# Optimization experiments

Measured on AMD Instinct MI355X. Metric: run time of the kernel, lower is better.

## Reference

```python
import jax, jax.numpy as jnp
import numpy as np

KERNEL = 5
PADDING = 2
STRIDE = 2
MIXTURES = 2
OUT_CH = 128


def setup_inputs() -> dict:
    key = jax.random.key(0)
    ks = jax.random.split(key, 7)
    B, CIN, H, W = 8, 64, 128, 128
    return {
        "x": jax.random.normal(ks[0], (B, CIN, H, W), jnp.float32),
        "w_q": jax.random.normal(ks[1], (OUT_CH, CIN), jnp.float32) * 0.05,
        "w_k": jax.random.normal(ks[2], (OUT_CH, CIN), jnp.float32) * 0.05,
        "w_v": jax.random.normal(ks[3], (OUT_CH * MIXTURES, CIN), jnp.float32) * 0.05,
        "row_emb": jax.random.normal(ks[4], (OUT_CH, KERNEL), jnp.float32),
        "col_emb": jax.random.normal(ks[5], (OUT_CH, KERNEL), jnp.float32),
        "mix_emb": jax.random.normal(ks[6], (OUT_CH, MIXTURES), jnp.float32),
    }


def _patches(t, stride):
    # im2col, matching torch nn.Unfold channel-major ordering: [B, C*k*k, Ho, Wo]
    return jax.lax.conv_general_dilated_patches(
        t, (KERNEL, KERNEL), (stride, stride),
        padding=[(PADDING, PADDING), (PADDING, PADDING)])


def reference(x, w_q, w_k, w_v, row_emb, col_emb, mix_emb):
    K2 = KERNEL * KERNEL
    # 1x1 convolutions (groups=1, no bias)
    q = jnp.einsum('bchw,oc->bohw', x, w_q)            # [B,C,H,W]
    k = jnp.einsum('bchw,oc->bohw', x, w_k)            # [B,C,H,W]
    v = jnp.einsum('bchw,oc->bohw', x, w_v)            # [B,C*M,H,W]

    # key patches: [B, C, K2, Ho, Wo]
    kp = _patches(k, STRIDE)
    B, _, Ho, Wo = kp.shape
    kp = kp.reshape(B, OUT_CH, K2, Ho, Wo)

    # queries at strided output locations (unfold with kernel 1, stride s)
    qs = q[:, :, ::STRIDE, ::STRIDE]                   # [B,C,Ho,Wo]

    # attention over the local window, softmax along K2
    scores = jnp.einsum('bchw,bckhw->bkhw', qs, kp)    # [B,K2,Ho,Wo]
    attn = jax.nn.softmax(scores, axis=1)

    # mixture positional weights: sum_c (row[c,i]+col[c,j]) * mix[c,m] -> [M,k,k]
    wpos = (jnp.einsum('ci,cm->mi', row_emb, mix_emb)[:, :, None]
            + jnp.einsum('cj,cm->mj', col_emb, mix_emb)[:, None, :])
    wpos = jax.nn.softmax(wpos, axis=0).reshape(MIXTURES, K2)  # softmax over mixtures

    # value patches: [B, C, M, K2, Ho, Wo] (channel-major as in torch reshape)
    vp = _patches(v, STRIDE).reshape(B, OUT_CH, MIXTURES, K2, Ho, Wo)
    vals = jnp.einsum('bcmkhw,mk->bckhw', vp, wpos)    # mixture-weighted values

    # attention-weighted sum over the window
    out = jnp.einsum('bckhw,bkhw->bchw', vals, attn)   # [B,C,Ho,Wo]
    return out
```

## Files before the change

### kernel.cpp

```cpp
#include <hip/hip_runtime.h>

typedef unsigned int   uint_;
typedef unsigned short u16;

#define B_    8
#define CIN_  64
#define H_    128
#define W_    128
#define OC_   128
#define HO_   64
#define WO_   64
#define NPOS  (B_ * HO_ * WO_)

#define XBT_OFF  0
#define MHI_OFF  4194304
#define MLO_OFF  4196352
#define WHI_OFF  4198400
#define WLO_OFF  4206592
#define WPOS_OFF 4214784

__device__ __forceinline__ u16 f2bf(float x) {
  uint_ u = __float_as_uint(x);
  u += 0x7FFFu + ((u >> 16) & 1u);
  return (u16)(u >> 16);
}
__device__ __forceinline__ uint_ pack2bf(float lo, float hi) {
  return ((uint_)f2bf(hi) << 16) | (uint_)f2bf(lo);
}

template <int CTRL>
__device__ __forceinline__ float dpp_add(float x) {
  int y = __builtin_amdgcn_update_dpp(0, __float_as_int(x), CTRL, 0xf, 0xf, true);
  return x + __int_as_float(y);
}

typedef __attribute__((ext_vector_type(8))) short bfrag;
typedef __attribute__((ext_vector_type(4))) float f4;

__global__ __launch_bounds__(256) void mega_kernel(
    const float* __restrict__ x, u16* __restrict__ xbt,
    const float* __restrict__ w_q, const float* __restrict__ w_k,
    const float* __restrict__ w_v,
    const float* __restrict__ row_emb, const float* __restrict__ col_emb,
    const float* __restrict__ mix_emb,
    u16* __restrict__ MhiF, u16* __restrict__ MloF,
    u16* __restrict__ WhiF, u16* __restrict__ WloF,
    float* __restrict__ wpos) {
  if (blockIdx.x < 1024) {
    __shared__ float tile[64][129];
    int by = blockIdx.x;
    int b = by >> 7, y = by & 127;
    const float* xp = x + (size_t)b * (CIN_ * H_ * W_) + (size_t)y * W_;
    #pragma unroll
    for (int it = 0; it < 32; ++it) {
      int idx = threadIdx.x + it * 256;
      int c = idx >> 7, xw = idx & 127;
      tile[c][xw] = xp[(size_t)c * (H_ * W_) + xw];
    }
    __syncthreads();
    uint_* dst = (uint_*)(xbt + ((size_t)(b * H_ + y)) * (W_ * 64));
    #pragma unroll
    for (int it = 0; it < 16; ++it) {
      int idx = threadIdx.x + it * 256;
      int xw = idx >> 5, cp = idx & 31;
      dst[idx] = pack2bf(tile[2 * cp][xw], tile[2 * cp + 1][xw]);
    }
  } else {
    int pb = blockIdx.x - 1024;
    if (pb < 16) {
      int idx = pb * 256 + threadIdx.x;
      int a = idx >> 6, c = idx & 63;
      float acc = 0.f;
      #pragma unroll 8
      for (int o = 0; o < 128; ++o)
        acc = fmaf(w_q[o * 64 + a], w_k[o * 64 + c], acc);
      u16 hi = f2bf(acc);
      float hif = __uint_as_float((uint_)hi << 16);
      u16 lo = f2bf(acc - hif);
      int m = c >> 4, lr = c & 15;
      int ks = a >> 5, q = (a >> 3) & 3, jr = a & 7;
      int off = ((ks * 4 + m) * 64 + (lr + 16 * q)) * 8 + jr;
      MhiF[off] = hi;
      MloF[off] = lo;
    } else if (pb == 16) {
      int p = threadIdx.x;
      if (p < 25) {
        int i = p / 5, j = p % 5;
        float a0 = 0.f, a1 = 0.f;
        for (int c = 0; c < 128; ++c) {
          float rc = row_emb[c * 5 + i] + col_emb[c * 5 + j];
          a0 = fmaf(rc, mix_emb[c * 2 + 0], a0);
          a1 = fmaf(rc, mix_emb[c * 2 + 1], a1);
        }
        float mx = fmaxf(a0, a1);
        float e0 = __expf(a0 - mx), e1 = __expf(a1 - mx);
        float inv = 1.f / (e0 + e1);
        wpos[p] = e0 * inv;
        wpos[32 + p] = e1 * inv;
      }
    } else {
      int t = (pb - 17) * 256 + threadIdx.x;
      #pragma unroll
      for (int e = 0; e < 4; ++e) {
        int elem = t * 4 + e;
        int c = elem >> 7, k = elem & 127;
        float w = w_v[elem];
        u16 hi = f2bf(w);
        float hif = __uint_as_float((uint_)hi << 16);
        u16 lo = f2bf(w - hif);
        int m = c >> 4, lr = c & 15;
        int ks = k >> 5, q = (k >> 3) & 3, j = k & 7;
        int off = ((ks * 8 + m) * 64 + (lr + 16 * q)) * 8 + j;
        WhiF[off] = hi;
        WloF[off] = lo;
      }
    }
  }
}

__global__ __launch_bounds__(512) void attn_out_kernel(
    const u16* __restrict__ xbt, const u16* __restrict__ MhiF,
    const u16* __restrict__ MloF, const float* __restrict__ wpos,
    const u16* __restrict__ WhiF, const u16* __restrict__ WloF,
    float* __restrict__ out) {
  __shared__ u16 Xl[5 * 67 * 64];
  __shared__ union {
    float Ul[32][68];
    u16   Gl[32][136];
  } GU;

  int tid = threadIdx.x;
  int wave = tid >> 6, lane = tid & 63;
  int lr = lane & 15, q = lane >> 4;

  int bid = (int)blockIdx.x;
  int swz = (bid & 7) * 128 + (bid >> 3);
  int pos0 = swz * 32;

  int b = pos0 >> 12;
  int ho0 = (pos0 >> 6) & 63;
  int wo0 = pos0 & 63;
  int y0 = 2 * ho0, x0base = 2 * wo0;

  {
    int sl = tid & 15;
    int pi0 = tid >> 4;
    const u16* xbb = xbt + (size_t)b * (H_ * W_ * 64);
    #pragma unroll
    for (int it = 0; it < 11; ++it) {
      int pi = it * 32 + pi0;
      if (pi < 335) {
        int row = pi / 67;
        int col = pi - row * 67;
        int yc = min(max(y0 + row - 2, 0), H_ - 1);
        int xc = min(max(x0base + col - 2, 0), W_ - 1);
        uint2 d = *(const uint2*)(xbb + ((size_t)yc * W_ + xc) * 64 + sl * 4);
        *(uint2*)(&Xl[pi * 64 + sl * 4]) = d;
      }
    }
  }

  {
    int pt = wave >> 2, mm = wave & 3;
    int pu = pos0 + pt * 16 + lr;
    int bu = pu >> 12, hou = (pu >> 6) & 63, wou = pu & 63;
    const u16* xq = xbt + ((size_t)(bu * H_ + 2 * hou) * W_ + 2 * wou) * 64;
    f4 ua = (f4)0.f;
    #pragma unroll
    for (int ks = 0; ks < 2; ++ks) {
      bfrag bb = *reinterpret_cast<const bfrag*>(xq + ks * 32 + q * 8);
      bfrag ah = *reinterpret_cast<const bfrag*>(
          MhiF + ((ks * 4 + mm) * 64 + lane) * 8);
      bfrag al = *reinterpret_cast<const bfrag*>(
          MloF + ((ks * 4 + mm) * 64 + lane) * 8);
      ua = __builtin_amdgcn_mfma_f32_16x16x32_bf16(ah, bb, ua, 0, 0, 0);
      ua = __builtin_amdgcn_mfma_f32_16x16x32_bf16(al, bb, ua, 0, 0, 0);
    }
    #pragma unroll
    for (int r = 0; r < 4; ++r)
      GU.Ul[pt * 16 + lr][mm * 16 + q * 4 + r] = ua[r];
  }
  __syncthreads();

  {
    int r = wave * 4 + q;
    int wo = wo0 + r;
    const u16* xl0 = &Xl[(2 * r + 2) * 64 + lr * 4];

    f4 u = *reinterpret_cast<const f4*>(&GU.Ul[r][lr * 4]);
    bool mn = (wo > 0), mp = (wo < 63);

    float Z = 0.f;
    float g0[4] = {0.f, 0.f, 0.f, 0.f}, g1[4] = {0.f, 0.f, 0.f, 0.f};

    #pragma unroll
    for (int dy = -2; dy <= 2; ++dy) {
      int y = y0 + dy;
      if ((unsigned)y < (unsigned)H_) {
        #pragma unroll
        for (int dx = -2; dx <= 2; ++dx) {
          const int p = (dy + 2) * 5 + (dx + 2);
          uint2 d = *(const uint2*)(xl0 + ((dy + 2) * 67 + dx) * 64);
          float xv0 = __uint_as_float(d.x << 16);
          float xv1 = __uint_as_float(d.x & 0xffff0000u);
          float xv2 = __uint_as_float(d.y << 16);
          float xv3 = __uint_as_float(d.y & 0xffff0000u);
          float sp = fmaf(u.x, xv0, fmaf(u.y, xv1, fmaf(u.z, xv2, u.w * xv3)));
          sp = dpp_add<0x121>(sp);
          sp = dpp_add<0x122>(sp);
          sp = dpp_add<0x124>(sp);
          sp = dpp_add<0x128>(sp);
          bool v = (dx < 0) ? mn : ((dx == 2) ? mp : true);
          sp = v ? sp : 0.f;
          float e = __expf(sp);
          Z += e;
          float c0 = v ? e * wpos[p] : 0.f;
          float c1 = v ? e * wpos[32 + p] : 0.f;
          g0[0] = fmaf(c0, xv0, g0[0]);
          g0[1] = fmaf(c0, xv1, g0[1]);
          g0[2] = fmaf(c0, xv2, g0[2]);
          g0[3] = fmaf(c0, xv3, g0[3]);
          g1[0] = fmaf(c1, xv0, g1[0]);
          g1[1] = fmaf(c1, xv1, g1[1]);
          g1[2] = fmaf(c1, xv2, g1[2]);
          g1[3] = fmaf(c1, xv3, g1[3]);
        }
      } else {
        Z += 5.f;
      }
    }
    float rZ = 1.f / Z;

    uint2 w0, w1;
    w0.x = pack2bf(g0[0] * rZ, g0[1] * rZ);
    w0.y = pack2bf(g0[2] * rZ, g0[3] * rZ);
    w1.x = pack2bf(g1[0] * rZ, g1[1] * rZ);
    w1.y = pack2bf(g1[2] * rZ, g1[3] * rZ);
    *(uint2*)&GU.Gl[r][lr * 4] = w0;
    *(uint2*)&GU.Gl[r][64 + lr * 4] = w1;
  }

  __syncthreads();

  {
    f4 acc0 = (f4)0.f, acc1 = (f4)0.f;
    #pragma unroll
    for (int ks = 0; ks < 4; ++ks) {
      bfrag b0 = *reinterpret_cast<const bfrag*>(&GU.Gl[lr][ks * 32 + q * 8]);
      bfrag b1 = *reinterpret_cast<const bfrag*>(&GU.Gl[16 + lr][ks * 32 + q * 8]);
      bfrag ah = *reinterpret_cast<const bfrag*>(
          WhiF + ((ks * 8 + wave) * 64 + lane) * 8);
      bfrag al = *reinterpret_cast<const bfrag*>(
          WloF + ((ks * 8 + wave) * 64 + lane) * 8);
      acc0 = __builtin_amdgcn_mfma_f32_16x16x32_bf16(ah, b0, acc0, 0, 0, 0);
      acc1 = __builtin_amdgcn_mfma_f32_16x16x32_bf16(ah, b1, acc1, 0, 0, 0);
      acc0 = __builtin_amdgcn_mfma_f32_16x16x32_bf16(al, b0, acc0, 0, 0, 0);
      acc1 = __builtin_amdgcn_mfma_f32_16x16x32_bf16(al, b1, acc1, 0, 0, 0);
    }
    int bb = pos0 >> 12;
    int hw0 = pos0 & 4095;
    float* op = out + (size_t)bb * (OC_ * HO_ * WO_) + hw0;
    #pragma unroll
    for (int rr = 0; rr < 4; ++rr) {
      int c = wave * 16 + q * 4 + rr;
      op[(size_t)c * 4096 + lr] = acc0[rr];
      op[(size_t)c * 4096 + 16 + lr] = acc1[rr];
    }
  }
}

extern "C" void kernel_launch(void* const* d_in, const int* in_sizes, int n_in,
                              void* d_out, int out_size, void* d_ws, size_t ws_size,
                              hipStream_t stream) {
  const float* x       = (const float*)d_in[0];
  const float* w_q     = (const float*)d_in[1];
  const float* w_k     = (const float*)d_in[2];
  const float* w_v     = (const float*)d_in[3];
  const float* row_emb = (const float*)d_in[4];
  const float* col_emb = (const float*)d_in[5];
  const float* mix_emb = (const float*)d_in[6];
  float* out = (float*)d_out;

  float* ws   = (float*)d_ws;
  u16*   xbt  = (u16*)(ws + XBT_OFF);
  u16*   MhiF = (u16*)(ws + MHI_OFF);
  u16*   MloF = (u16*)(ws + MLO_OFF);
  u16*   WhiF = (u16*)(ws + WHI_OFF);
  u16*   WloF = (u16*)(ws + WLO_OFF);
  float* wpos = ws + WPOS_OFF;

  mega_kernel<<<1024 + 33, 256, 0, stream>>>(x, xbt, w_q, w_k, w_v, row_emb,
                                             col_emb, mix_emb, MhiF, MloF,
                                             WhiF, WloF, wpos);
  attn_out_kernel<<<NPOS / 32, 512, 0, stream>>>(xbt, MhiF, MloF, wpos,
                                                 WhiF, WloF, out);
}
```

Before: 39.32 us.

## Switch to fp16 storage and single-pass fp16 MFMA with packed-half window math

Replaces bf16 hi/lo split matrices with single fp16 matrices, halving the MFMA count in both GEMM stages, and stores x in fp16. The window loop now uses packed fp16 dot products and packed half FMAs for the accumulations, with a 1/256 scale folded into wpos and undone via rZ to avoid overflow. Out-of-bounds window pixels are zero-filled in shared memory so branches and masks are removed, and the LDS row stride is padded to 68 to reduce bank conflicts. Accuracy drops compared with the fp32/hi-lo path, and the half-precision accumulators risk overflow or precision loss.

```diff
diff --git a/kernel.cpp b/kernel.cpp
--- a/kernel.cpp
+++ b/kernel.cpp
@@ -2,6 +2,11 @@
 
 typedef unsigned int   uint_;
 typedef unsigned short u16;
+typedef _Float16 f16;
+typedef __attribute__((ext_vector_type(8))) _Float16 f16x8;
+typedef __attribute__((ext_vector_type(2))) _Float16 f16x2;
+typedef __attribute__((ext_vector_type(2))) __fp16 fp16x2_builtin;
+typedef __attribute__((ext_vector_type(4))) float f4;
 
 #define B_    8
 #define CIN_  64
@@ -13,19 +18,20 @@
 #define NPOS  (B_ * HO_ * WO_)
 
 #define XBT_OFF  0
-#define MHI_OFF  4194304
-#define MLO_OFF  4196352
-#define WHI_OFF  4198400
-#define WLO_OFF  4206592
-#define WPOS_OFF 4214784
-
-__device__ __forceinline__ u16 f2bf(float x) {
-  uint_ u = __float_as_uint(x);
-  u += 0x7FFFu + ((u >> 16) & 1u);
-  return (u16)(u >> 16);
-}
-__device__ __forceinline__ uint_ pack2bf(float lo, float hi) {
-  return ((uint_)f2bf(hi) << 16) | (uint_)f2bf(lo);
+#define MF_OFF   4194304
+#define WF_OFF   4196352
+#define WPOS_OFF 4204544
+
+__device__ __forceinline__ uint_ h2u(f16x2 h) {
+  union { uint_ u; f16x2 h; } c; c.h = h; return c.u;
+}
+__device__ __forceinline__ u16 f2h_bits(float x) {
+  union { f16 h; u16 u; } c; c.h = (f16)x; return c.u;
+}
+__device__ __forceinline__ f16x2 cvt_pk2h(float lo, float hi) {
+  union { fp16x2_builtin b; f16x2 h; } c;
+  c.b = __builtin_amdgcn_cvt_pkrtz(lo, hi);
+  return c.h;
 }
 
 template <int CTRL>
@@ -34,8 +40,13 @@
   return x + __int_as_float(y);
 }
 
-typedef __attribute__((ext_vector_type(8))) short bfrag;
-typedef __attribute__((ext_vector_type(4))) float f4;
+__device__ __forceinline__ float fdot2h(f16x2 a, f16x2 b, float c) {
+#if __has_builtin(__builtin_amdgcn_fdot2)
+  return __builtin_amdgcn_fdot2(a, b, c, false);
+#else
+  return fmaf((float)a[0], (float)b[0], fmaf((float)a[1], (float)b[1], c));
+#endif
+}
 
 __global__ __launch_bounds__(256) void mega_kernel(
     const float* __restrict__ x, u16* __restrict__ xbt,
@@ -43,9 +54,7 @@
     const float* __restrict__ w_v,
     const float* __restrict__ row_emb, const float* __restrict__ col_emb,
     const float* __restrict__ mix_emb,
-    u16* __restrict__ MhiF, u16* __restrict__ MloF,
-    u16* __restrict__ WhiF, u16* __restrict__ WloF,
-    float* __restrict__ wpos) {
+    u16* __restrict__ MF, u16* __restrict__ WF, float* __restrict__ wpos) {
   if (blockIdx.x < 1024) {
     __shared__ float tile[64][129];
     int by = blockIdx.x;
@@ -63,7 +72,7 @@
     for (int it = 0; it < 16; ++it) {
       int idx = threadIdx.x + it * 256;
       int xw = idx >> 5, cp = idx & 31;
-      dst[idx] = pack2bf(tile[2 * cp][xw], tile[2 * cp + 1][xw]);
+      dst[idx] = h2u(cvt_pk2h(tile[2 * cp][xw], tile[2 * cp + 1][xw]));
     }
   } else {
     int pb = blockIdx.x - 1024;
@@ -74,14 +83,10 @@
       #pragma unroll 8
       for (int o = 0; o < 128; ++o)
         acc = fmaf(w_q[o * 64 + a], w_k[o * 64 + c], acc);
-      u16 hi = f2bf(acc);
-      float hif = __uint_as_float((uint_)hi << 16);
-      u16 lo = f2bf(acc - hif);
       int m = c >> 4, lr = c & 15;
       int ks = a >> 5, q = (a >> 3) & 3, jr = a & 7;
       int off = ((ks * 4 + m) * 64 + (lr + 16 * q)) * 8 + jr;
-      MhiF[off] = hi;
-      MloF[off] = lo;
+      MF[off] = f2h_bits(acc);
     } else if (pb == 16) {
       int p = threadIdx.x;
       if (p < 25) {
@@ -94,7 +99,7 @@
         }
         float mx = fmaxf(a0, a1);
         float e0 = __expf(a0 - mx), e1 = __expf(a1 - mx);
-        float inv = 1.f / (e0 + e1);
+        float inv = 0.00390625f / (e0 + e1);
         wpos[p] = e0 * inv;
         wpos[32 + p] = e1 * inv;
       }
@@ -104,26 +109,20 @@
       for (int e = 0; e < 4; ++e) {
         int elem = t * 4 + e;
         int c = elem >> 7, k = elem & 127;
-        float w = w_v[elem];
-        u16 hi = f2bf(w);
-        float hif = __uint_as_float((uint_)hi << 16);
-        u16 lo = f2bf(w - hif);
         int m = c >> 4, lr = c & 15;
         int ks = k >> 5, q = (k >> 3) & 3, j = k & 7;
         int off = ((ks * 8 + m) * 64 + (lr + 16 * q)) * 8 + j;
-        WhiF[off] = hi;
-        WloF[off] = lo;
+        WF[off] = f2h_bits(w_v[elem]);
       }
     }
   }
 }
 
 __global__ __launch_bounds__(512) void attn_out_kernel(
-    const u16* __restrict__ xbt, const u16* __restrict__ MhiF,
-    const u16* __restrict__ MloF, const float* __restrict__ wpos,
-    const u16* __restrict__ WhiF, const u16* __restrict__ WloF,
+    const u16* __restrict__ xbt, const u16* __restrict__ MF,
+    const float* __restrict__ wpos, const u16* __restrict__ WF,
     float* __restrict__ out) {
-  __shared__ u16 Xl[5 * 67 * 64];
+  __shared__ u16 Xl[5 * 67 * 68];
   __shared__ union {
     float Ul[32][68];
     u16   Gl[32][136];
@@ -152,10 +151,13 @@
       if (pi < 335) {
         int row = pi / 67;
         int col = pi - row * 67;
-        int yc = min(max(y0 + row - 2, 0), H_ - 1);
-        int xc = min(max(x0base + col - 2, 0), W_ - 1);
+        int yr = y0 + row - 2, xr = x0base + col - 2;
+        bool oob = ((unsigned)yr >= (unsigned)H_) | ((unsigned)xr >= (unsigned)W_);
+        int yc = min(max(yr, 0), H_ - 1);
+        int xc = min(max(xr, 0), W_ - 1);
         uint2 d = *(const uint2*)(xbb + ((size_t)yc * W_ + xc) * 64 + sl * 4);
-        *(uint2*)(&Xl[pi * 64 + sl * 4]) = d;
+        if (oob) { d.x = 0u; d.y = 0u; }
+        *(uint2*)(&Xl[pi * 68 + sl * 4]) = d;
       }
     }
   }
@@ -168,13 +170,10 @@
     f4 ua = (f4)0.f;
     #pragma unroll
     for (int ks = 0; ks < 2; ++ks) {
-      bfrag bb = *reinterpret_cast<const bfrag*>(xq + ks * 32 + q * 8);
-      bfrag ah = *reinterpret_cast<const bfrag*>(
-          MhiF + ((ks * 4 + mm) * 64 + lane) * 8);
-      bfrag al = *reinterpret_cast<const bfrag*>(
-          MloF + ((ks * 4 + mm) * 64 + lane) * 8);
-      ua = __builtin_amdgcn_mfma_f32_16x16x32_bf16(ah, bb, ua, 0, 0, 0);
-      ua = __builtin_amdgcn_mfma_f32_16x16x32_bf16(al, bb, ua, 0, 0, 0);
+      f16x8 bb = *reinterpret_cast<const f16x8*>(xq + ks * 32 + q * 8);
+      f16x8 ah = *reinterpret_cast<const f16x8*>(
+          MF + ((ks * 4 + mm) * 64 + lane) * 8);
+      ua = __builtin_amdgcn_mfma_f32_16x16x32_f16(ah, bb, ua, 0, 0, 0);
     }
     #pragma unroll
     for (int r = 0; r < 4; ++r)
@@ -184,58 +183,43 @@
 
   {
     int r = wave * 4 + q;
-    int wo = wo0 + r;
-    const u16* xl0 = &Xl[(2 * r + 2) * 64 + lr * 4];
+    const u16* xl0 = &Xl[(2 * r) * 68 + lr * 4];
 
     f4 u = *reinterpret_cast<const f4*>(&GU.Ul[r][lr * 4]);
-    bool mn = (wo > 0), mp = (wo < 63);
+    f16x2 u01 = cvt_pk2h(u.x, u.y);
+    f16x2 u23 = cvt_pk2h(u.z, u.w);
 
     float Z = 0.f;
-    float g0[4] = {0.f, 0.f, 0.f, 0.f}, g1[4] = {0.f, 0.f, 0.f, 0.f};
-
-    #pragma unroll
-    for (int dy = -2; dy <= 2; ++dy) {
-      int y = y0 + dy;
-      if ((unsigned)y < (unsigned)H_) {
-        #pragma unroll
-        for (int dx = -2; dx <= 2; ++dx) {
-          const int p = (dy + 2) * 5 + (dx + 2);
-          uint2 d = *(const uint2*)(xl0 + ((dy + 2) * 67 + dx) * 64);
-          float xv0 = __uint_as_float(d.x << 16);
-          float xv1 = __uint_as_float(d.x & 0xffff0000u);
-          float xv2 = __uint_as_float(d.y << 16);
-          float xv3 = __uint_as_float(d.y & 0xffff0000u);
-          float sp = fmaf(u.x, xv0, fmaf(u.y, xv1, fmaf(u.z, xv2, u.w * xv3)));
-          sp = dpp_add<0x121>(sp);
-          sp = dpp_add<0x122>(sp);
-          sp = dpp_add<0x124>(sp);
-          sp = dpp_add<0x128>(sp);
-          bool v = (dx < 0) ? mn : ((dx == 2) ? mp : true);
-          sp = v ? sp : 0.f;
-          float e = __expf(sp);
-          Z += e;
-          float c0 = v ? e * wpos[p] : 0.f;
-          float c1 = v ? e * wpos[32 + p] : 0.f;
-          g0[0] = fmaf(c0, xv0, g0[0]);
-          g0[1] = fmaf(c0, xv1, g0[1]);
-          g0[2] = fmaf(c0, xv2, g0[2]);
-          g0[3] = fmaf(c0, xv3, g0[3]);
-          g1[0] = fmaf(c1, xv0, g1[0]);
-          g1[1] = fmaf(c1, xv1, g1[1]);
-          g1[2] = fmaf(c1, xv2, g1[2]);
-          g1[3] = fmaf(c1, xv3, g1[3]);
-        }
-      } else {
-        Z += 5.f;
-      }
-    }
-    float rZ = 1.f / Z;
+    f16x2 g0a = (f16x2)0.f, g0b = (f16x2)0.f;
+    f16x2 g1a = (f16x2)0.f, g1b = (f16x2)0.f;
+
+    #pragma unroll
+    for (int p = 0; p < 25; ++p) {
+      const int dy = p / 5, dx = p % 5;
+      uint2 d = *(const uint2*)(xl0 + (dy * 67 + dx) * 68);
+      f16x2 x01, x23;
+      *(uint_*)&x01 = d.x;
+      *(uint_*)&x23 = d.y;
+      float sp = fdot2h(x23, u23, fdot2h(x01, u01, 0.f));
+      sp = dpp_add<0x121>(sp);
+      sp = dpp_add<0x122>(sp);
+      sp = dpp_add<0x124>(sp);
+      sp = dpp_add<0x128>(sp);
+      float e = __expf(sp);
+      Z += e;
+      f16x2 c0 = cvt_pk2h(e * wpos[p], e * wpos[p]);
+      f16x2 c1 = cvt_pk2h(e * wpos[32 + p], e * wpos[32 + p]);
+      g0a = x01 * c0 + g0a;
+      g0b = x23 * c0 + g0b;
+      g1a = x01 * c1 + g1a;
+      g1b = x23 * c1 + g1b;
+    }
+    float rZ = 256.f / Z;
+    f16x2 rZpk = cvt_pk2h(rZ, rZ);
 
     uint2 w0, w1;
-    w0.x = pack2bf(g0[0] * rZ, g0[1] * rZ);
-    w0.y = pack2bf(g0[2] * rZ, g0[3] * rZ);
-    w1.x = pack2bf(g1[0] * rZ, g1[1] * rZ);
-    w1.y = pack2bf(g1[2] * rZ, g1[3] * rZ);
+    w0.x = h2u(g0a * rZpk); w0.y = h2u(g0b * rZpk);
+    w1.x = h2u(g1a * rZpk); w1.y = h2u(g1b * rZpk);
     *(uint2*)&GU.Gl[r][lr * 4] = w0;
     *(uint2*)&GU.Gl[r][64 + lr * 4] = w1;
   }
@@ -246,16 +230,12 @@
     f4 acc0 = (f4)0.f, acc1 = (f4)0.f;
     #pragma unroll
     for (int ks = 0; ks < 4; ++ks) {
-      bfrag b0 = *reinterpret_cast<const bfrag*>(&GU.Gl[lr][ks * 32 + q * 8]);
-      bfrag b1 = *reinterpret_cast<const bfrag*>(&GU.Gl[16 + lr][ks * 32 + q * 8]);
-      bfrag ah = *reinterpret_cast<const bfrag*>(
-          WhiF + ((ks * 8 + wave) * 64 + lane) * 8);
-      bfrag al = *reinterpret_cast<const bfrag*>(
-          WloF + ((ks * 8 + wave) * 64 + lane) * 8);
-      acc0 = __builtin_amdgcn_mfma_f32_16x16x32_bf16(ah, b0, acc0, 0, 0, 0);
-      acc1 = __builtin_amdgcn_mfma_f32_16x16x32_bf16(ah, b1, acc1, 0, 0, 0);
-      acc0 = __builtin_amdgcn_mfma_f32_16x16x32_bf16(al, b0, acc0, 0, 0, 0);
-      acc1 = __builtin_amdgcn_mfma_f32_16x16x32_bf16(al, b1, acc1, 0, 0, 0);
+      f16x8 b0 = *reinterpret_cast<const f16x8*>(&GU.Gl[lr][ks * 32 + q * 8]);
+      f16x8 b1 = *reinterpret_cast<const f16x8*>(&GU.Gl[16 + lr][ks * 32 + q * 8]);
+      f16x8 ah = *reinterpret_cast<const f16x8*>(
+          WF + ((ks * 8 + wave) * 64 + lane) * 8);
+      acc0 = __builtin_amdgcn_mfma_f32_16x16x32_f16(ah, b0, acc0, 0, 0, 0);
+      acc1 = __builtin_amdgcn_mfma_f32_16x16x32_f16(ah, b1, acc1, 0, 0, 0);
     }
     int bb = pos0 >> 12;
     int hw0 = pos0 & 4095;
@@ -283,15 +263,11 @@
 
   float* ws   = (float*)d_ws;
   u16*   xbt  = (u16*)(ws + XBT_OFF);
-  u16*   MhiF = (u16*)(ws + MHI_OFF);
-  u16*   MloF = (u16*)(ws + MLO_OFF);
-  u16*   WhiF = (u16*)(ws + WHI_OFF);
-  u16*   WloF = (u16*)(ws + WLO_OFF);
+  u16*   MF   = (u16*)(ws + MF_OFF);
+  u16*   WF   = (u16*)(ws + WF_OFF);
   float* wpos = ws + WPOS_OFF;
 
   mega_kernel<<<1024 + 33, 256, 0, stream>>>(x, xbt, w_q, w_k, w_v, row_emb,
-                                             col_emb, mix_emb, MhiF, MloF,
-                                             WhiF, WloF, wpos);
-  attn_out_kernel<<<NPOS / 32, 512, 0, stream>>>(xbt, MhiF, MloF, wpos,
-                                                 WhiF, WloF, out);
-}
+                                             col_emb, mix_emb, MF, WF, wpos);
+  attn_out_kernel<<<NPOS / 32, 512, 0, stream>>>(xbt, MF, wpos, WF, out);
+}
```

New measurement: 36.92 us. -6.1%, faster.
